# Performance work log

Hardware: AMD Instinct MI355X
Metric: run time of the kernel (lower is better)

The kernel has to match this reference:

```python
import jax, jax.numpy as jnp
import numpy as np

N_NODES = 100000
N_EDGES = 1600000
NFEAT = 128
NHID = 64


def setup_inputs() -> dict:
    key = jax.random.key(0)
    k1, k2, k3, k4 = jax.random.split(key, 4)
    x = jax.random.normal(k1, (N_NODES, NFEAT), dtype=jnp.float32)
    edge_index = jax.random.randint(k2, (2, N_EDGES), 0, N_NODES, dtype=jnp.int64)
    # Glorot-ish scaled weights
    W1 = jax.random.normal(k3, (NFEAT, NHID), dtype=jnp.float32) * (1.0 / np.sqrt(NFEAT))
    b1 = jnp.zeros((NHID,), dtype=jnp.float32)
    W2 = jax.random.normal(k4, (NHID, NFEAT), dtype=jnp.float32) * (1.0 / np.sqrt(NHID))
    b2 = jnp.zeros((NFEAT,), dtype=jnp.float32)
    return {"x": x, "edge_index": edge_index, "W1": W1, "b1": b1, "W2": W2, "b2": b2}


def _gcn_norm(edge_index, num_nodes):
    # PyG GCNConv default: add self-loops, symmetric normalization D^-1/2 A D^-1/2
    src, dst = edge_index[0], edge_index[1]
    loops = jnp.arange(num_nodes, dtype=src.dtype)
    src = jnp.concatenate([src, loops])
    dst = jnp.concatenate([dst, loops])
    ones = jnp.ones(src.shape[0], dtype=jnp.float32)
    deg = jax.ops.segment_sum(ones, dst, num_segments=num_nodes)  # in-degree incl. self-loop
    dinv = jax.lax.rsqrt(deg)  # deg >= 1 due to self-loops
    norm = dinv[src] * dinv[dst]  # [E + N]
    return src, dst, norm


def _gcn_conv(h, W, b, src, dst, norm, num_nodes):
    h = h @ W                                  # [N, d_out] transform first (d_out small)
    msg = norm[:, None] * h[src]               # gather over edges [E+N, d_out]
    out = jax.ops.segment_sum(msg, dst, num_segments=num_nodes)  # scatter-add
    return out + b


def reference(x, edge_index, W1, b1, W2, b2):
    num_nodes = x.shape[0]
    src, dst, norm = _gcn_norm(edge_index, num_nodes)
    h = jax.nn.relu(_gcn_conv(x, W1, b1, src, dst, norm, num_nodes))
    # dropout is identity in eval mode (deterministic reference baseline)
    out = _gcn_conv(h, W2, b2, src, dst, norm, num_nodes)
    return out
```

## Files before the change

kernel.cpp:

```cpp
#include <hip/hip_runtime.h>
#include <hip/hip_fp16.h>

#define NFEAT 128
#define NHID 64
#define MAXB 1024
#define BSHIFT 8
#define BNODES 256
#define PBLK 512
#define DBINS 512

typedef _Float16 f16x8 __attribute__((ext_vector_type(8)));
typedef float f32x4 __attribute__((ext_vector_type(4)));

__global__ void k_detect(const int* __restrict__ ei_words, int nwords, int* flag,
                         const float* __restrict__ W1, __half* __restrict__ w1t,
                         const float* __restrict__ W2, __half* __restrict__ w2t) {
    __shared__ int s_or;
    if (threadIdx.x == 0) s_or = 0;
    __syncthreads();
    int acc = 0;
    for (int i = 1 + 2 * (int)threadIdx.x; i < nwords; i += 2 * (int)blockDim.x)
        acc |= ei_words[i];
    atomicOr(&s_or, acc);
    for (int i = threadIdx.x; i < NFEAT * NHID; i += 256) {
        int n = i >> 7, k = i & 127;
        w1t[i] = __float2half(W1[k * NHID + n]);
    }
    for (int i = threadIdx.x; i < NFEAT * NHID; i += 256) {
        int n = i >> 6, k = i & 63;
        w2t[i] = __float2half(W2[k * NFEAT + n]);
    }
    __syncthreads();
    if (threadIdx.x == 0) *flag = (s_or == 0) ? 1 : 0;
}

__device__ __forceinline__ int edge_idx(const int* __restrict__ ei, int is64,
                                        long long E, long long e, int which) {
    long long pos = which ? (E + e) : e;
    return is64 ? ei[2 * pos] : ei[pos];
}

__device__ __forceinline__ void load8(const int* __restrict__ ei, int is64,
                                      long long E, long long e0, int which,
                                      int (&v)[8]) {
    if (is64) {
        const int* base = ei + 2 * (which ? E + e0 : e0);
        int4 a = *(const int4*)(base + 0);
        int4 b = *(const int4*)(base + 4);
        int4 c = *(const int4*)(base + 8);
        int4 d = *(const int4*)(base + 12);
        v[0] = a.x; v[1] = a.z; v[2] = b.x; v[3] = b.z;
        v[4] = c.x; v[5] = c.z; v[6] = d.x; v[7] = d.z;
    } else {
        const int* base = ei + (which ? E + e0 : e0);
        int4 a = *(const int4*)(base + 0);
        int4 b = *(const int4*)(base + 4);
        v[0] = a.x; v[1] = a.y; v[2] = a.z; v[3] = a.w;
        v[4] = b.x; v[5] = b.y; v[6] = b.z; v[7] = b.w;
    }
}

__global__ __launch_bounds__(256) void k_bhist(const int* __restrict__ ei,
                                               const int* __restrict__ flag,
                                               long long E, int* gbhist,
                                               int* __restrict__ blockhist,
                                               int NB, long long perblk) {
    __shared__ int hist[MAXB];
    for (int i = threadIdx.x; i < NB; i += 256) hist[i] = 0;
    __syncthreads();
    int is64 = *flag;
    long long lo = (long long)blockIdx.x * perblk;
    long long hi = lo + perblk; if (hi > E) hi = E;
    for (long long e0 = lo + (long long)threadIdx.x * 8; e0 + 8 <= hi; e0 += 256 * 8) {
        int d[8];
        load8(ei, is64, E, e0, 1, d);
#pragma unroll
        for (int j = 0; j < 8; ++j)
            atomicAdd(&hist[d[j] >> BSHIFT], 1);
    }
    long long tail = lo + ((hi - lo) & ~7LL);
    for (long long e = tail + threadIdx.x; e < hi; e += 256) {
        int d = edge_idx(ei, is64, E, e, 1);
        atomicAdd(&hist[d >> BSHIFT], 1);
    }
    __syncthreads();
    int* bh = blockhist + (size_t)blockIdx.x * MAXB;
    for (int i = threadIdx.x; i < NB; i += 256) {
        int v = hist[i];
        bh[i] = v;
        if (v) atomicAdd(&gbhist[i], v);
    }
}

__global__ __launch_bounds__(256) void k_bscan(const int* __restrict__ gbhist, int NB,
                                               int* boff, int* bcur, int* offN) {
    __shared__ int s[256];
    int t = threadIdx.x;
    int v[4]; int sum = 0;
#pragma unroll
    for (int j = 0; j < 4; ++j) {
        int i = t * 4 + j;
        v[j] = (i < NB) ? gbhist[i] : 0;
        sum += v[j];
    }
    s[t] = sum;
    __syncthreads();
    for (int d = 1; d < 256; d <<= 1) {
        int val = (t >= d) ? s[t - d] : 0;
        __syncthreads();
        s[t] += val;
        __syncthreads();
    }
    int run = s[t] - sum;
#pragma unroll
    for (int j = 0; j < 4; ++j) {
        int i = t * 4 + j;
        if (i <= NB) boff[i] = run;
        if (i < NB)  bcur[i] = run;
        run += v[j];
    }
    if (t == 255) *offN = s[255];
}

__global__ __launch_bounds__(256) void k_partition(const int* __restrict__ ei,
                                                   const int* __restrict__ flag,
                                                   long long E, int* bcur,
                                                   const int* __restrict__ blockhist,
                                                   unsigned* __restrict__ staging,
                                                   int NB, long long perblk) {
    __shared__ int cur[MAXB];
    const int* bh = blockhist + (size_t)blockIdx.x * MAXB;
    for (int i = threadIdx.x; i < NB; i += 256) {
        int v = bh[i];
        cur[i] = v ? atomicAdd(&bcur[i], v) : 0;
    }
    __syncthreads();
    long long lo = (long long)blockIdx.x * perblk;
    long long hi = lo + perblk; if (hi > E) hi = E;
    int is64 = *flag;
    for (long long e0 = lo + (long long)threadIdx.x * 8; e0 + 8 <= hi; e0 += 256 * 8) {
        int s[8], d[8];
        load8(ei, is64, E, e0, 0, s);
        load8(ei, is64, E, e0, 1, d);
#pragma unroll
        for (int j = 0; j < 8; ++j) {
            int pos = atomicAdd(&cur[d[j] >> BSHIFT], 1);
            staging[pos] = (unsigned)s[j] | ((unsigned)(d[j] & (BNODES - 1)) << 24);
        }
    }
    long long tail = lo + ((hi - lo) & ~7LL);
    for (long long e = tail + threadIdx.x; e < hi; e += 256) {
        int s = edge_idx(ei, is64, E, e, 0);
        int d = edge_idx(ei, is64, E, e, 1);
        int pos = atomicAdd(&cur[d >> BSHIFT], 1);
        staging[pos] = (unsigned)s | ((unsigned)(d & (BNODES - 1)) << 24);
    }
}

__global__ __launch_bounds__(256) void k_bucket(const unsigned* __restrict__ staging,
                                                const int* __restrict__ boff,
                                                int N, int* off, int* esrc, float* dinv,
                                                int* __restrict__ deghist) {
    __shared__ int cnt_s[BNODES];
    __shared__ int scan_s[BNODES];
    __shared__ int dh[DBINS];
    int b = blockIdx.x;
    int base = b << BSHIFT;
    int t = threadIdx.x;
    cnt_s[t] = 0;
    dh[t] = 0; dh[t + 256] = 0;
    __syncthreads();
    int lo = boff[b], hi = boff[b + 1];
    for (int e = lo + t; e < hi; e += 256)
        atomicAdd(&cnt_s[staging[e] >> 24], 1);
    __syncthreads();
    int v = cnt_s[t];
    scan_s[t] = v;
    __syncthreads();
    for (int d = 1; d < 256; d <<= 1) {
        int val = (t >= d) ? scan_s[t - d] : 0;
        __syncthreads();
        scan_s[t] += val;
        __syncthreads();
    }
    int excl = scan_s[t] - v;
    int node = base + t;
    if (node < N) {
        off[node] = lo + excl;
        dinv[node] = rsqrtf((float)v + 1.0f);
        atomicAdd(&dh[v < (DBINS - 1) ? v : (DBINS - 1)], 1);
    }
    __syncthreads();
    if (dh[t])       atomicAdd(&deghist[t], dh[t]);
    if (dh[t + 256]) atomicAdd(&deghist[t + 256], dh[t + 256]);
    cnt_s[t] = lo + excl;
    __syncthreads();
    for (int e = lo + t; e < hi; e += 256) {
        unsigned sd = staging[e];
        int pos = atomicAdd(&cnt_s[sd >> 24], 1);
        esrc[pos] = (int)(sd & 0xFFFFFFu);
    }
}

__global__ __launch_bounds__(256) void k_dscan(const int* __restrict__ deghist, int* dcur) {
    __shared__ int s[256];
    int t = threadIdx.x;
    int v0 = deghist[2 * t], v1 = deghist[2 * t + 1];
    int sum = v0 + v1;
    s[t] = sum;
    __syncthreads();
    for (int d = 1; d < 256; d <<= 1) {
        int val = (t >= d) ? s[t - d] : 0;
        __syncthreads();
        s[t] += val;
        __syncthreads();
    }
    int run = s[t] - sum;
    dcur[2 * t] = run;
    dcur[2 * t + 1] = run + v0;
}

__global__ __launch_bounds__(256) void k_dperm(const int* __restrict__ off, int* dcur,
                                               int* __restrict__ perm, int N) {
    __shared__ int cnt[DBINS];
    __shared__ int base[DBINS];
    int t = threadIdx.x;
    cnt[t] = 0; cnt[t + 256] = 0;
    __syncthreads();
    int n = blockIdx.x * 256 + t;
    int b = 0, myidx = 0;
    if (n < N) {
        int deg = off[n + 1] - off[n];
        b = deg < (DBINS - 1) ? deg : (DBINS - 1);
        myidx = atomicAdd(&cnt[b], 1);
    }
    __syncthreads();
    int c0 = cnt[t];       if (c0) base[t] = atomicAdd(&dcur[t], c0);
    int c1 = cnt[t + 256]; if (c1) base[t + 256] = atomicAdd(&dcur[t + 256], c1);
    __syncthreads();
    if (n < N) perm[base[b] + myidx] = n;
}

__device__ __forceinline__ int swz(int row, int byteoff) {
    return (row << 8) + (byteoff ^ ((row & 7) << 4));
}
__device__ __forceinline__ int swz64(int row, int byteoff) {
    return (row << 7) + (byteoff ^ ((row & 7) << 4));
}

__global__ __launch_bounds__(256) void k_gemm1(const float* __restrict__ x,
                                               const __half* __restrict__ w1t,
                                               const float* __restrict__ dinv,
                                               __half* __restrict__ xw1s, int N) {
    __shared__ __align__(16) __half xs[64 * NFEAT];
    __shared__ __align__(16) __half ws[NHID * NFEAT];
    int t = threadIdx.x;
    for (int i = t; i < NHID * NFEAT / 8; i += 256) {
        int row = i >> 4, c16 = (i & 15) << 4;
        uint4 v = ((const uint4*)w1t)[i];
        *(uint4*)((char*)ws + swz(row, c16)) = v;
    }
    int row0 = blockIdx.x * 64;
    for (int i = t; i < 64 * 32; i += 256) {
        int r = i >> 5, c4 = i & 31;
        int row = row0 + r;
        float4 v = (row < N) ? ((const float4*)x)[(size_t)row * 32 + c4]
                             : make_float4(0.f, 0.f, 0.f, 0.f);
        __half2 h0 = __floats2half2_rn(v.x, v.y);
        __half2 h1 = __floats2half2_rn(v.z, v.w);
        uint2 p = make_uint2(*(unsigned*)&h0, *(unsigned*)&h1);
        *(uint2*)((char*)xs + swz(r, c4 * 8)) = p;
    }
    __syncthreads();
    int wave = t >> 6, lane = t & 63;
    int lr = lane & 15, g = lane >> 4;
    int xrow = wave * 16 + lr;
    f16x8 xb[4];
#pragma unroll
    for (int kc = 0; kc < 4; ++kc)
        xb[kc] = *(const f16x8*)((const char*)xs + swz(xrow, kc * 64 + g * 16));
    int row = row0 + xrow;
    float di = (row < N) ? dinv[row] : 0.f;
#pragma unroll
    for (int c = 0; c < 4; ++c) {
        f32x4 acc = {0.f, 0.f, 0.f, 0.f};
#pragma unroll
        for (int kc = 0; kc < 4; ++kc) {
            f16x8 a = *(const f16x8*)((const char*)ws + swz(c * 16 + lr, kc * 64 + g * 16));
            acc = __builtin_amdgcn_mfma_f32_16x16x32_f16(a, xb[kc], acc, 0, 0, 0);
        }
        if (row < N) {
            __half2 o0 = __floats2half2_rn(di * acc[0], di * acc[1]);
            __half2 o1 = __floats2half2_rn(di * acc[2], di * acc[3]);
            uint2 p = make_uint2(*(unsigned*)&o0, *(unsigned*)&o1);
            *(uint2*)&xw1s[(size_t)row * NHID + c * 16 + g * 4] = p;
        }
    }
}

__device__ __forceinline__ void addhalf8(float2 (&acc)[4], uint4 p) {
    const __half2* hh = (const __half2*)&p;
#pragma unroll
    for (int j = 0; j < 4; ++j) {
        float2 v = __half22float2(hh[j]);
        acc[j].x += v.x; acc[j].y += v.y;
    }
}

__device__ __forceinline__ void gather_group(const int* __restrict__ off,
                                             const int* __restrict__ esrc,
                                             const uint4* __restrict__ feat4,
                                             int d, int li, int lo, int hi,
                                             float2 (&acc)[4]) {
#pragma unroll
    for (int j = 0; j < 4; ++j) acc[j] = make_float2(0.f, 0.f);
    int idx = (lo + li < hi) ? esrc[lo + li] : 0;
    for (int e = lo; e < hi; e += 8) {
        int nrem = hi - e;
        int cur = idx;
        int ne = e + 8;
        idx = (ne + li < hi) ? esrc[ne + li] : 0;
        if (nrem >= 8) {
#pragma unroll
            for (int j = 0; j < 8; ++j) {
                int s = __shfl(cur, j, 8);
                addhalf8(acc, feat4[(size_t)s * 8 + li]);
            }
        } else {
            for (int j = 0; j < nrem; ++j) {
                int s = __shfl(cur, j, 8);
                addhalf8(acc, feat4[(size_t)s * 8 + li]);
            }
        }
    }
    addhalf8(acc, feat4[(size_t)d * 8 + li]);
}

__global__ __launch_bounds__(256) void k_agg1(const int* __restrict__ off,
                                              const int* __restrict__ esrc,
                                              const int* __restrict__ perm,
                                              const float* __restrict__ dinv,
                                              const uint4* __restrict__ xw1s4,
                                              const float* __restrict__ b1,
                                              uint4* __restrict__ h4, int N) {
    int t = threadIdx.x;
    int lane = t & 63, wave = t >> 6;
    int g = lane >> 3, li = lane & 7;
    int slot = blockIdx.x * 32 + wave * 8 + g;
    bool valid = slot < N;
    int d  = valid ? perm[slot] : 0;
    int lo = valid ? off[d] : 0;
    int hi = valid ? off[d + 1] : 0;
    float2 acc[4];
    gather_group(off, esrc, xw1s4, d, li, lo, hi, acc);
    float dd = dinv[d];
    float4 bA = ((const float4*)b1)[li * 2 + 0];
    float4 bB = ((const float4*)b1)[li * 2 + 1];
    float v0 = fmaxf(dd * acc[0].x + bA.x, 0.f);
    float v1 = fmaxf(dd * acc[0].y + bA.y, 0.f);
    float v2 = fmaxf(dd * acc[1].x + bA.z, 0.f);
    float v3 = fmaxf(dd * acc[1].y + bA.w, 0.f);
    float v4 = fmaxf(dd * acc[2].x + bB.x, 0.f);
    float v5 = fmaxf(dd * acc[2].y + bB.y, 0.f);
    float v6 = fmaxf(dd * acc[3].x + bB.z, 0.f);
    float v7 = fmaxf(dd * acc[3].y + bB.w, 0.f);
    __half2 o[4];
    o[0] = __floats2half2_rn(dd * v0, dd * v1);
    o[1] = __floats2half2_rn(dd * v2, dd * v3);
    o[2] = __floats2half2_rn(dd * v4, dd * v5);
    o[3] = __floats2half2_rn(dd * v6, dd * v7);
    if (valid) h4[(size_t)d * 8 + li] = *(const uint4*)o;
}

__global__ __launch_bounds__(256) void k_agg2(const int* __restrict__ off,
                                              const int* __restrict__ esrc,
                                              const int* __restrict__ perm,
                                              const float* __restrict__ dinv,
                                              const uint4* __restrict__ h4,
                                              uint4* __restrict__ a2h,
                                              uint4* __restrict__ a2l, int N) {
    int t = threadIdx.x;
    int lane = t & 63, wave = t >> 6;
    int g = lane >> 3, li = lane & 7;
    int slot = blockIdx.x * 32 + wave * 8 + g;
    bool valid = slot < N;
    int d  = valid ? perm[slot] : 0;
    int lo = valid ? off[d] : 0;
    int hi = valid ? off[d + 1] : 0;
    float2 acc[4];
    gather_group(off, esrc, h4, d, li, lo, hi, acc);
    float dd = dinv[d];
    float v[8] = {dd * acc[0].x, dd * acc[0].y, dd * acc[1].x, dd * acc[1].y,
                  dd * acc[2].x, dd * acc[2].y, dd * acc[3].x, dd * acc[3].y};
    __half hh[8], ll[8];
#pragma unroll
    for (int j = 0; j < 8; ++j) {
        hh[j] = __float2half(v[j]);
        ll[j] = __float2half(v[j] - __half2float(hh[j]));
    }
    uint4 ph, pl;
    __half2* hp = (__half2*)&ph;
    __half2* lp = (__half2*)&pl;
#pragma unroll
    for (int j = 0; j < 4; ++j) {
        hp[j] = __halves2half2(hh[2 * j], hh[2 * j + 1]);
        lp[j] = __halves2half2(ll[2 * j], ll[2 * j + 1]);
    }
    if (valid) {
        a2h[(size_t)d * 8 + li] = ph;
        a2l[(size_t)d * 8 + li] = pl;
    }
}

__global__ __launch_bounds__(256) void k_gemm2(const __half* __restrict__ a2h,
                                               const __half* __restrict__ a2l,
                                               const __half* __restrict__ w2t,
                                               const float* __restrict__ b2,
                                               float* __restrict__ out, int N) {
    __shared__ __align__(16) __half sB[NFEAT * NHID];
    __shared__ __align__(16) __half sH[64 * NHID];
    __shared__ __align__(16) __half sL[64 * NHID];
    int t = threadIdx.x;
    for (int i = t; i < NFEAT * NHID / 8; i += 256) {
        int row = i >> 3, c16 = (i & 7) << 4;
        uint4 v = ((const uint4*)w2t)[i];
        *(uint4*)((char*)sB + swz64(row, c16)) = v;
    }
    int row0 = blockIdx.x * 64;
    for (int i = t; i < 64 * 8; i += 256) {
        int r = i >> 3, c16 = (i & 7) << 4;
        int row = row0 + r;
        uint4 vh = make_uint4(0, 0, 0, 0), vl = make_uint4(0, 0, 0, 0);
        if (row < N) {
            vh = *(const uint4*)((const char*)a2h + (size_t)row * 128 + c16);
            vl = *(const uint4*)((const char*)a2l + (size_t)row * 128 + c16);
        }
        *(uint4*)((char*)sH + swz64(r, c16)) = vh;
        *(uint4*)((char*)sL + swz64(r, c16)) = vl;
    }
    __syncthreads();
    int wave = t >> 6, lane = t & 63;
    int lr = lane & 15, g = lane >> 4;
    int xrow = wave * 16 + lr;
    f16x8 xh[2], xl[2];
#pragma unroll
    for (int kc = 0; kc < 2; ++kc) {
        xh[kc] = *(const f16x8*)((const char*)sH + swz64(xrow, kc * 64 + g * 16));
        xl[kc] = *(const f16x8*)((const char*)sL + swz64(xrow, kc * 64 + g * 16));
    }
    int row = row0 + xrow;
#pragma unroll
    for (int c = 0; c < 8; ++c) {
        f32x4 acc = {0.f, 0.f, 0.f, 0.f};
#pragma unroll
        for (int kc = 0; kc < 2; ++kc) {
            f16x8 a = *(const f16x8*)((const char*)sB + swz64(c * 16 + lr, kc * 64 + g * 16));
            acc = __builtin_amdgcn_mfma_f32_16x16x32_f16(a, xl[kc], acc, 0, 0, 0);
            acc = __builtin_amdgcn_mfma_f32_16x16x32_f16(a, xh[kc], acc, 0, 0, 0);
        }
        if (row < N) {
            float4 bb = *(const float4*)&b2[c * 16 + g * 4];
            float4 o = make_float4(acc[0] + bb.x, acc[1] + bb.y,
                                   acc[2] + bb.z, acc[3] + bb.w);
            *(float4*)&out[(size_t)row * NFEAT + c * 16 + g * 4] = o;
        }
    }
}

static inline char* align256(char* p) {
    return (char*)(((uintptr_t)p + 255) & ~(uintptr_t)255);
}

extern "C" void kernel_launch(void* const* d_in, const int* in_sizes, int n_in,
                              void* d_out, int out_size, void* d_ws, size_t ws_size,
                              hipStream_t stream) {
    const float* x  = (const float*)d_in[0];
    const int*   ei = (const int*)d_in[1];
    const float* W1 = (const float*)d_in[2];
    const float* b1 = (const float*)d_in[3];
    const float* W2 = (const float*)d_in[4];
    const float* b2 = (const float*)d_in[5];
    float* out = (float*)d_out;

    const int N = in_sizes[0] / NFEAT;
    const long long E = in_sizes[1] / 2;
    const int NB = (N + BNODES - 1) >> BSHIFT;

    char* w = (char*)d_ws;
    int*      flag      = (int*)w;
    int*      gbhist    = (int*)(w + 256);
    int*      boff      = gbhist + MAXB;
    int*      bcur      = boff + MAXB + 1;
    int*      deghist   = bcur + MAXB;
    int*      dcur      = deghist + DBINS;
    int*      blockhist = dcur + DBINS;
    float*    dinv      = (float*)(blockhist + (size_t)PBLK * MAXB);
    int*      off       = (int*)(dinv + N);
    int*      perm      = off + N + 1;
    char*     p         = align256((char*)(perm + N));
    unsigned* staging   = (unsigned*)p;
    p = align256((char*)(staging + E));
    int*      esrc      = (int*)p;
    p = align256((char*)(esrc + E));
    __half*   xw1s      = (__half*)p;
    p = align256((char*)(xw1s + (size_t)N * NHID));
    __half*   h         = (__half*)p;
    p = align256((char*)(h + (size_t)N * NHID));
    __half*   a2h       = (__half*)p;
    p = align256((char*)(a2h + (size_t)N * NHID));
    __half*   a2l       = (__half*)p;
    p = align256((char*)(a2l + (size_t)N * NHID));
    __half*   w1t       = (__half*)p;
    p = align256((char*)(w1t + NFEAT * NHID));
    __half*   w2t       = (__half*)p;

    hipMemsetAsync(gbhist, 0, (size_t)NB * sizeof(int), stream);
    hipMemsetAsync(deghist, 0, (size_t)DBINS * sizeof(int), stream);

    long long perblk = ((E + PBLK - 1) / PBLK + 7) & ~7LL;
    k_detect<<<1, 256, 0, stream>>>(ei, 4096, flag, W1, w1t, W2, w2t);
    k_bhist<<<PBLK, 256, 0, stream>>>(ei, flag, E, gbhist, blockhist, NB, perblk);
    k_bscan<<<1, 256, 0, stream>>>(gbhist, NB, boff, bcur, off + N);
    k_partition<<<PBLK, 256, 0, stream>>>(ei, flag, E, bcur, blockhist, staging, NB, perblk);
    k_bucket<<<NB, 256, 0, stream>>>(staging, boff, N, off, esrc, dinv, deghist);
    k_dscan<<<1, 256, 0, stream>>>(deghist, dcur);
    k_dperm<<<(N + 255) / 256, 256, 0, stream>>>(off, dcur, perm, N);

    k_gemm1<<<(N + 63) / 64, 256, 0, stream>>>(x, w1t, dinv, xw1s, N);

    k_agg1<<<(N + 31) / 32, 256, 0, stream>>>(off, esrc, perm, dinv, (const uint4*)xw1s,
                                              b1, (uint4*)h, N);
    k_agg2<<<(N + 31) / 32, 256, 0, stream>>>(off, esrc, perm, dinv, (const uint4*)h,
                                              (uint4*)a2h, (uint4*)a2l, N);

    k_gemm2<<<(N + 63) / 64, 256, 0, stream>>>(a2h, a2l, w2t, b2, out, N);
}
```

Measured before the change: 303.8 us.

## Fuse CSR preprocessing into one cooperative kernel with grid syncs

Replaces the seven preprocessing kernels and two memsets with a single cooperative kernel that moves between phases with grid.sync(). A fallback chain of separate kernels runs if the cooperative launch fails. Global atomics on bucket cursors are replaced by a deterministic column scan over per-block histograms. Weight transposition moves into the GEMM kernels, each of which converts fp32 weights with scattered half stores. The aim is to cut launch and inter-kernel gaps; the trade-offs are grid-sync cost, limited occupancy at 2 blocks/SM, and the bucket and dperm phases now looping over 512 blocks.

```diff
diff --git a/kernel.cpp b/kernel.cpp
--- a/kernel.cpp
+++ b/kernel.cpp
@@ -1,5 +1,8 @@
 #include <hip/hip_runtime.h>
 #include <hip/hip_fp16.h>
+#include <hip/hip_cooperative_groups.h>
+
+namespace cg = cooperative_groups;
 
 #define NFEAT 128
 #define NHID 64
@@ -12,27 +15,6 @@
 typedef _Float16 f16x8 __attribute__((ext_vector_type(8)));
 typedef float f32x4 __attribute__((ext_vector_type(4)));
 
-__global__ void k_detect(const int* __restrict__ ei_words, int nwords, int* flag,
-                         const float* __restrict__ W1, __half* __restrict__ w1t,
-                         const float* __restrict__ W2, __half* __restrict__ w2t) {
-    __shared__ int s_or;
-    if (threadIdx.x == 0) s_or = 0;
-    __syncthreads();
-    int acc = 0;
-    for (int i = 1 + 2 * (int)threadIdx.x; i < nwords; i += 2 * (int)blockDim.x)
-        acc |= ei_words[i];
-    atomicOr(&s_or, acc);
-    for (int i = threadIdx.x; i < NFEAT * NHID; i += 256) {
-        int n = i >> 7, k = i & 127;
-        w1t[i] = __float2half(W1[k * NHID + n]);
-    }
-    for (int i = threadIdx.x; i < NFEAT * NHID; i += 256) {
-        int n = i >> 6, k = i & 63;
-        w2t[i] = __float2half(W2[k * NFEAT + n]);
-    }
-    __syncthreads();
-    if (threadIdx.x == 0) *flag = (s_or == 0) ? 1 : 0;
-}
 
 __device__ __forceinline__ int edge_idx(const int* __restrict__ ei, int is64,
                                         long long E, long long e, int which) {
@@ -60,41 +42,79 @@
     }
 }
 
-__global__ __launch_bounds__(256) void k_bhist(const int* __restrict__ ei,
-                                               const int* __restrict__ flag,
-                                               long long E, int* gbhist,
-                                               int* __restrict__ blockhist,
-                                               int NB, long long perblk) {
-    __shared__ int hist[MAXB];
+__device__ __forceinline__ int block_is64(const int* __restrict__ ei, int* smem) {
+    if (threadIdx.x == 0) smem[0] = 0;
+    __syncthreads();
+    int acc = 0;
+    for (int i = 1 + 2 * (int)threadIdx.x; i < 4096; i += 512)
+        acc |= ei[i];
+    atomicOr(&smem[0], acc);
+    __syncthreads();
+    int r = (smem[0] == 0) ? 1 : 0;
+    __syncthreads();
+    return r;
+}
+
+__device__ void phase_hist(const int* __restrict__ ei, int is64, long long E,
+                           long long perblk, int* __restrict__ blockhist,
+                           int NB, int* smem) {
+    int* hist = smem;
     for (int i = threadIdx.x; i < NB; i += 256) hist[i] = 0;
     __syncthreads();
-    int is64 = *flag;
     long long lo = (long long)blockIdx.x * perblk;
     long long hi = lo + perblk; if (hi > E) hi = E;
-    for (long long e0 = lo + (long long)threadIdx.x * 8; e0 + 8 <= hi; e0 += 256 * 8) {
-        int d[8];
-        load8(ei, is64, E, e0, 1, d);
-#pragma unroll
-        for (int j = 0; j < 8; ++j)
-            atomicAdd(&hist[d[j] >> BSHIFT], 1);
-    }
-    long long tail = lo + ((hi - lo) & ~7LL);
-    for (long long e = tail + threadIdx.x; e < hi; e += 256) {
-        int d = edge_idx(ei, is64, E, e, 1);
-        atomicAdd(&hist[d >> BSHIFT], 1);
+    if (lo < hi) {
+        for (long long e0 = lo + (long long)threadIdx.x * 8; e0 + 8 <= hi; e0 += 256 * 8) {
+            int d[8];
+            load8(ei, is64, E, e0, 1, d);
+#pragma unroll
+            for (int j = 0; j < 8; ++j)
+                atomicAdd(&hist[d[j] >> BSHIFT], 1);
+        }
+        long long tail = lo + ((hi - lo) & ~7LL);
+        for (long long e = tail + threadIdx.x; e < hi; e += 256) {
+            int d = edge_idx(ei, is64, E, e, 1);
+            atomicAdd(&hist[d >> BSHIFT], 1);
+        }
     }
     __syncthreads();
     int* bh = blockhist + (size_t)blockIdx.x * MAXB;
-    for (int i = threadIdx.x; i < NB; i += 256) {
-        int v = hist[i];
-        bh[i] = v;
-        if (v) atomicAdd(&gbhist[i], v);
-    }
-}
-
-__global__ __launch_bounds__(256) void k_bscan(const int* __restrict__ gbhist, int NB,
-                                               int* boff, int* bcur, int* offN) {
-    __shared__ int s[256];
+    for (int i = threadIdx.x; i < NB; i += 256) bh[i] = hist[i];
+    __syncthreads();
+}
+
+__device__ void phase_colscan(int* __restrict__ blockhist, int* __restrict__ gbhist,
+                              int* __restrict__ deghist, int NB, int* smem) {
+    int b = blockIdx.x;
+    int t = threadIdx.x;
+    if (b < NB) {
+        int v0 = blockhist[(size_t)(2 * t) * MAXB + b];
+        int v1 = blockhist[(size_t)(2 * t + 1) * MAXB + b];
+        int sum = v0 + v1;
+        int* s = smem;
+        s[t] = sum;
+        __syncthreads();
+        for (int d = 1; d < 256; d <<= 1) {
+            int val = (t >= d) ? s[t - d] : 0;
+            __syncthreads();
+            s[t] += val;
+            __syncthreads();
+        }
+        int run = s[t] - sum;
+        blockhist[(size_t)(2 * t) * MAXB + b] = run;
+        blockhist[(size_t)(2 * t + 1) * MAXB + b] = run + v0;
+        if (t == 255) gbhist[b] = s[255];
+        __syncthreads();
+    } else {
+        int idx = (b - NB) * 256 + t;
+        if (idx < DBINS) deghist[idx] = 0;
+    }
+}
+
+__device__ void phase_bscan(const int* __restrict__ gbhist, int NB,
+                            int* __restrict__ boff, int* __restrict__ offN,
+                            int* smem) {
+    int* s = smem;
     int t = threadIdx.x;
     int v[4]; int sum = 0;
 #pragma unroll
@@ -116,94 +136,96 @@
     for (int j = 0; j < 4; ++j) {
         int i = t * 4 + j;
         if (i <= NB) boff[i] = run;
-        if (i < NB)  bcur[i] = run;
         run += v[j];
     }
     if (t == 255) *offN = s[255];
-}
-
-__global__ __launch_bounds__(256) void k_partition(const int* __restrict__ ei,
-                                                   const int* __restrict__ flag,
-                                                   long long E, int* bcur,
-                                                   const int* __restrict__ blockhist,
-                                                   unsigned* __restrict__ staging,
-                                                   int NB, long long perblk) {
-    __shared__ int cur[MAXB];
+    __syncthreads();
+}
+
+__device__ void phase_partition(const int* __restrict__ ei, int is64, long long E,
+                                long long perblk, const int* __restrict__ boff,
+                                const int* __restrict__ blockhist,
+                                unsigned* __restrict__ staging, int NB, int* smem) {
+    int* cur = smem;
     const int* bh = blockhist + (size_t)blockIdx.x * MAXB;
-    for (int i = threadIdx.x; i < NB; i += 256) {
-        int v = bh[i];
-        cur[i] = v ? atomicAdd(&bcur[i], v) : 0;
-    }
+    for (int i = threadIdx.x; i < NB; i += 256)
+        cur[i] = boff[i] + bh[i];
     __syncthreads();
     long long lo = (long long)blockIdx.x * perblk;
     long long hi = lo + perblk; if (hi > E) hi = E;
-    int is64 = *flag;
-    for (long long e0 = lo + (long long)threadIdx.x * 8; e0 + 8 <= hi; e0 += 256 * 8) {
-        int s[8], d[8];
-        load8(ei, is64, E, e0, 0, s);
-        load8(ei, is64, E, e0, 1, d);
-#pragma unroll
-        for (int j = 0; j < 8; ++j) {
-            int pos = atomicAdd(&cur[d[j] >> BSHIFT], 1);
-            staging[pos] = (unsigned)s[j] | ((unsigned)(d[j] & (BNODES - 1)) << 24);
-        }
-    }
-    long long tail = lo + ((hi - lo) & ~7LL);
-    for (long long e = tail + threadIdx.x; e < hi; e += 256) {
-        int s = edge_idx(ei, is64, E, e, 0);
-        int d = edge_idx(ei, is64, E, e, 1);
-        int pos = atomicAdd(&cur[d >> BSHIFT], 1);
-        staging[pos] = (unsigned)s | ((unsigned)(d & (BNODES - 1)) << 24);
-    }
-}
-
-__global__ __launch_bounds__(256) void k_bucket(const unsigned* __restrict__ staging,
-                                                const int* __restrict__ boff,
-                                                int N, int* off, int* esrc, float* dinv,
-                                                int* __restrict__ deghist) {
-    __shared__ int cnt_s[BNODES];
-    __shared__ int scan_s[BNODES];
-    __shared__ int dh[DBINS];
-    int b = blockIdx.x;
-    int base = b << BSHIFT;
-    int t = threadIdx.x;
-    cnt_s[t] = 0;
-    dh[t] = 0; dh[t + 256] = 0;
-    __syncthreads();
-    int lo = boff[b], hi = boff[b + 1];
-    for (int e = lo + t; e < hi; e += 256)
-        atomicAdd(&cnt_s[staging[e] >> 24], 1);
-    __syncthreads();
-    int v = cnt_s[t];
-    scan_s[t] = v;
-    __syncthreads();
-    for (int d = 1; d < 256; d <<= 1) {
-        int val = (t >= d) ? scan_s[t - d] : 0;
-        __syncthreads();
-        scan_s[t] += val;
-        __syncthreads();
-    }
-    int excl = scan_s[t] - v;
-    int node = base + t;
-    if (node < N) {
-        off[node] = lo + excl;
-        dinv[node] = rsqrtf((float)v + 1.0f);
-        atomicAdd(&dh[v < (DBINS - 1) ? v : (DBINS - 1)], 1);
-    }
-    __syncthreads();
-    if (dh[t])       atomicAdd(&deghist[t], dh[t]);
-    if (dh[t + 256]) atomicAdd(&deghist[t + 256], dh[t + 256]);
-    cnt_s[t] = lo + excl;
-    __syncthreads();
-    for (int e = lo + t; e < hi; e += 256) {
-        unsigned sd = staging[e];
-        int pos = atomicAdd(&cnt_s[sd >> 24], 1);
-        esrc[pos] = (int)(sd & 0xFFFFFFu);
-    }
-}
-
-__global__ __launch_bounds__(256) void k_dscan(const int* __restrict__ deghist, int* dcur) {
-    __shared__ int s[256];
+    if (lo < hi) {
+        for (long long e0 = lo + (long long)threadIdx.x * 8; e0 + 8 <= hi; e0 += 256 * 8) {
+            int s[8], d[8];
+            load8(ei, is64, E, e0, 0, s);
+            load8(ei, is64, E, e0, 1, d);
+#pragma unroll
+            for (int j = 0; j < 8; ++j) {
+                int pos = atomicAdd(&cur[d[j] >> BSHIFT], 1);
+                staging[pos] = (unsigned)s[j] | ((unsigned)(d[j] & (BNODES - 1)) << 24);
+            }
+        }
+        long long tail = lo + ((hi - lo) & ~7LL);
+        for (long long e = tail + threadIdx.x; e < hi; e += 256) {
+            int s = edge_idx(ei, is64, E, e, 0);
+            int d = edge_idx(ei, is64, E, e, 1);
+            int pos = atomicAdd(&cur[d >> BSHIFT], 1);
+            staging[pos] = (unsigned)s | ((unsigned)(d & (BNODES - 1)) << 24);
+        }
+    }
+    __syncthreads();
+}
+
+__device__ void phase_bucket(const unsigned* __restrict__ staging,
+                             const int* __restrict__ boff, int N, int NB,
+                             int* __restrict__ off, int* __restrict__ esrc,
+                             float* __restrict__ dinv, int* __restrict__ deghist,
+                             int* smem) {
+    int* cnt_s  = smem;
+    int* scan_s = smem + 256;
+    int* dh     = smem + 512;
+    int t = threadIdx.x;
+    for (int b = blockIdx.x; b < NB; b += PBLK) {
+        int base = b << BSHIFT;
+        cnt_s[t] = 0;
+        dh[t] = 0; dh[t + 256] = 0;
+        __syncthreads();
+        int lo = boff[b], hi = boff[b + 1];
+        for (int e = lo + t; e < hi; e += 256)
+            atomicAdd(&cnt_s[staging[e] >> 24], 1);
+        __syncthreads();
+        int v = cnt_s[t];
+        scan_s[t] = v;
+        __syncthreads();
+        for (int d = 1; d < 256; d <<= 1) {
+            int val = (t >= d) ? scan_s[t - d] : 0;
+            __syncthreads();
+            scan_s[t] += val;
+            __syncthreads();
+        }
+        int excl = scan_s[t] - v;
+        int node = base + t;
+        if (node < N) {
+            off[node] = lo + excl;
+            dinv[node] = rsqrtf((float)v + 1.0f);
+            atomicAdd(&dh[v < (DBINS - 1) ? v : (DBINS - 1)], 1);
+        }
+        __syncthreads();
+        if (dh[t])       atomicAdd(&deghist[t], dh[t]);
+        if (dh[t + 256]) atomicAdd(&deghist[t + 256], dh[t + 256]);
+        cnt_s[t] = lo + excl;
+        __syncthreads();
+        for (int e = lo + t; e < hi; e += 256) {
+            unsigned sd = staging[e];
+            int pos = atomicAdd(&cnt_s[sd >> 24], 1);
+            esrc[pos] = (int)(sd & 0xFFFFFFu);
+        }
+        __syncthreads();
+    }
+}
+
+__device__ void phase_dscan(const int* __restrict__ deghist, int* __restrict__ dcur,
+                            int* smem) {
+    int* s = smem;
     int t = threadIdx.x;
     int v0 = deghist[2 * t], v1 = deghist[2 * t + 1];
     int sum = v0 + v1;
@@ -218,27 +240,93 @@
     int run = s[t] - sum;
     dcur[2 * t] = run;
     dcur[2 * t + 1] = run + v0;
-}
-
-__global__ __launch_bounds__(256) void k_dperm(const int* __restrict__ off, int* dcur,
-                                               int* __restrict__ perm, int N) {
-    __shared__ int cnt[DBINS];
-    __shared__ int base[DBINS];
-    int t = threadIdx.x;
-    cnt[t] = 0; cnt[t + 256] = 0;
-    __syncthreads();
-    int n = blockIdx.x * 256 + t;
-    int b = 0, myidx = 0;
-    if (n < N) {
-        int deg = off[n + 1] - off[n];
-        b = deg < (DBINS - 1) ? deg : (DBINS - 1);
-        myidx = atomicAdd(&cnt[b], 1);
-    }
-    __syncthreads();
-    int c0 = cnt[t];       if (c0) base[t] = atomicAdd(&dcur[t], c0);
-    int c1 = cnt[t + 256]; if (c1) base[t + 256] = atomicAdd(&dcur[t + 256], c1);
-    __syncthreads();
-    if (n < N) perm[base[b] + myidx] = n;
+    __syncthreads();
+}
+
+__device__ void phase_dperm(const int* __restrict__ off, int* __restrict__ dcur,
+                            int* __restrict__ perm, int N, int* smem) {
+    int* cnt  = smem;
+    int* base = smem + 512;
+    int t = threadIdx.x;
+    for (long long n0 = (long long)blockIdx.x * 256; n0 < N; n0 += (long long)PBLK * 256) {
+        cnt[t] = 0; cnt[t + 256] = 0;
+        __syncthreads();
+        int n = (int)n0 + t;
+        int b = 0, myidx = 0;
+        if (n < N) {
+            int deg = off[n + 1] - off[n];
+            b = deg < (DBINS - 1) ? deg : (DBINS - 1);
+            myidx = atomicAdd(&cnt[b], 1);
+        }
+        __syncthreads();
+        int c0 = cnt[t];       if (c0) base[t] = atomicAdd(&dcur[t], c0);
+        int c1 = cnt[t + 256]; if (c1) base[t + 256] = atomicAdd(&dcur[t + 256], c1);
+        __syncthreads();
+        if (n < N) perm[base[b] + myidx] = n;
+        __syncthreads();
+    }
+}
+
+__global__ __launch_bounds__(256, 2) void k_preproc_coop(
+        const int* __restrict__ ei, long long E, int N, int NB, long long perblk,
+        int* blockhist, int* gbhist, int* boff, unsigned* staging,
+        int* off, int* esrc, float* dinv, int* deghist, int* dcur, int* perm) {
+    __shared__ int smem[1024];
+    cg::grid_group grid = cg::this_grid();
+    int is64 = block_is64(ei, smem);
+    phase_hist(ei, is64, E, perblk, blockhist, NB, smem);
+    grid.sync();
+    phase_colscan(blockhist, gbhist, deghist, NB, smem);
+    grid.sync();
+    if (blockIdx.x == 0) phase_bscan(gbhist, NB, boff, off + N, smem);
+    grid.sync();
+    phase_partition(ei, is64, E, perblk, boff, blockhist, staging, NB, smem);
+    grid.sync();
+    phase_bucket(staging, boff, N, NB, off, esrc, dinv, deghist, smem);
+    grid.sync();
+    if (blockIdx.x == 0) phase_dscan(deghist, dcur, smem);
+    grid.sync();
+    phase_dperm(off, dcur, perm, N, smem);
+}
+
+__global__ __launch_bounds__(256) void k_f_hist(const int* __restrict__ ei, long long E,
+                                                long long perblk, int* blockhist, int NB) {
+    __shared__ int smem[1024];
+    int is64 = block_is64(ei, smem);
+    phase_hist(ei, is64, E, perblk, blockhist, NB, smem);
+}
+__global__ __launch_bounds__(256) void k_f_colscan(int* blockhist, int* gbhist,
+                                                   int* deghist, int NB) {
+    __shared__ int smem[1024];
+    phase_colscan(blockhist, gbhist, deghist, NB, smem);
+}
+__global__ __launch_bounds__(256) void k_f_bscan(const int* gbhist, int NB,
+                                                 int* boff, int* offN) {
+    __shared__ int smem[1024];
+    phase_bscan(gbhist, NB, boff, offN, smem);
+}
+__global__ __launch_bounds__(256) void k_f_partition(const int* __restrict__ ei, long long E,
+                                                     long long perblk, const int* boff,
+                                                     const int* blockhist,
+                                                     unsigned* staging, int NB) {
+    __shared__ int smem[1024];
+    int is64 = block_is64(ei, smem);
+    phase_partition(ei, is64, E, perblk, boff, blockhist, staging, NB, smem);
+}
+__global__ __launch_bounds__(256) void k_f_bucket(const unsigned* staging, const int* boff,
+                                                  int N, int NB, int* off, int* esrc,
+                                                  float* dinv, int* deghist) {
+    __shared__ int smem[1024];
+    phase_bucket(staging, boff, N, NB, off, esrc, dinv, deghist, smem);
+}
+__global__ __launch_bounds__(256) void k_f_dscan(const int* deghist, int* dcur) {
+    __shared__ int smem[1024];
+    phase_dscan(deghist, dcur, smem);
+}
+__global__ __launch_bounds__(256) void k_f_dperm(const int* off, int* dcur,
+                                                 int* perm, int N) {
+    __shared__ int smem[1024];
+    phase_dperm(off, dcur, perm, N, smem);
 }
 
 __device__ __forceinline__ int swz(int row, int byteoff) {
@@ -249,16 +337,15 @@
 }
 
 __global__ __launch_bounds__(256) void k_gemm1(const float* __restrict__ x,
-                                               const __half* __restrict__ w1t,
+                                               const float* __restrict__ W1,
                                                const float* __restrict__ dinv,
                                                __half* __restrict__ xw1s, int N) {
     __shared__ __align__(16) __half xs[64 * NFEAT];
     __shared__ __align__(16) __half ws[NHID * NFEAT];
     int t = threadIdx.x;
-    for (int i = t; i < NHID * NFEAT / 8; i += 256) {
-        int row = i >> 4, c16 = (i & 15) << 4;
-        uint4 v = ((const uint4*)w1t)[i];
-        *(uint4*)((char*)ws + swz(row, c16)) = v;
+    for (int i = t; i < NFEAT * NHID; i += 256) {
+        int k = i >> 6, n = i & 63;
+        *(__half*)((char*)ws + swz(n, k * 2)) = __float2half(W1[i]);
     }
     int row0 = blockIdx.x * 64;
     for (int i = t; i < 64 * 32; i += 256) {
@@ -414,17 +501,16 @@
 
 __global__ __launch_bounds__(256) void k_gemm2(const __half* __restrict__ a2h,
                                                const __half* __restrict__ a2l,
-                                               const __half* __restrict__ w2t,
+                                               const float* __restrict__ W2,
                                                const float* __restrict__ b2,
                                                float* __restrict__ out, int N) {
     __shared__ __align__(16) __half sB[NFEAT * NHID];
     __shared__ __align__(16) __half sH[64 * NHID];
     __shared__ __align__(16) __half sL[64 * NHID];
     int t = threadIdx.x;
-    for (int i = t; i < NFEAT * NHID / 8; i += 256) {
-        int row = i >> 3, c16 = (i & 7) << 4;
-        uint4 v = ((const uint4*)w2t)[i];
-        *(uint4*)((char*)sB + swz64(row, c16)) = v;
+    for (int i = t; i < NFEAT * NHID; i += 256) {
+        int k = i >> 7, n = i & 127;
+        *(__half*)((char*)sB + swz64(n, k * 2)) = __float2half(W2[i]);
     }
     int row0 = blockIdx.x * 64;
     for (int i = t; i < 64 * 8; i += 256) {
@@ -487,11 +573,9 @@
     const int NB = (N + BNODES - 1) >> BSHIFT;
 
     char* w = (char*)d_ws;
-    int*      flag      = (int*)w;
-    int*      gbhist    = (int*)(w + 256);
+    int*      gbhist    = (int*)w;
     int*      boff      = gbhist + MAXB;
-    int*      bcur      = boff + MAXB + 1;
-    int*      deghist   = bcur + MAXB;
+    int*      deghist   = boff + MAXB + 1;
     int*      dcur      = deghist + DBINS;
     int*      blockhist = dcur + DBINS;
     float*    dinv      = (float*)(blockhist + (size_t)PBLK * MAXB);
@@ -509,29 +593,41 @@
     __half*   a2h       = (__half*)p;
     p = align256((char*)(a2h + (size_t)N * NHID));
     __half*   a2l       = (__half*)p;
-    p = align256((char*)(a2l + (size_t)N * NHID));
-    __half*   w1t       = (__half*)p;
-    p = align256((char*)(w1t + NFEAT * NHID));
-    __half*   w2t       = (__half*)p;
-
-    hipMemsetAsync(gbhist, 0, (size_t)NB * sizeof(int), stream);
-    hipMemsetAsync(deghist, 0, (size_t)DBINS * sizeof(int), stream);
 
     long long perblk = ((E + PBLK - 1) / PBLK + 7) & ~7LL;
-    k_detect<<<1, 256, 0, stream>>>(ei, 4096, flag, W1, w1t, W2, w2t);
-    k_bhist<<<PBLK, 256, 0, stream>>>(ei, flag, E, gbhist, blockhist, NB, perblk);
-    k_bscan<<<1, 256, 0, stream>>>(gbhist, NB, boff, bcur, off + N);
-    k_partition<<<PBLK, 256, 0, stream>>>(ei, flag, E, bcur, blockhist, staging, NB, perblk);
-    k_bucket<<<NB, 256, 0, stream>>>(staging, boff, N, off, esrc, dinv, deghist);
-    k_dscan<<<1, 256, 0, stream>>>(deghist, dcur);
-    k_dperm<<<(N + 255) / 256, 256, 0, stream>>>(off, dcur, perm, N);
-
-    k_gemm1<<<(N + 63) / 64, 256, 0, stream>>>(x, w1t, dinv, xw1s, N);
+
+    {
+        const int* ei_ = ei; long long E_ = E; int N_ = N; int NB_ = NB;
+        long long pb_ = perblk;
+        int* blockhist_ = blockhist; int* gbhist_ = gbhist; int* boff_ = boff;
+        unsigned* staging_ = staging; int* off_ = off; int* esrc_ = esrc;
+        float* dinv_ = dinv; int* deghist_ = deghist; int* dcur_ = dcur;
+        int* perm_ = perm;
+        void* args[] = {&ei_, &E_, &N_, &NB_, &pb_, &blockhist_, &gbhist_, &boff_,
+                        &staging_, &off_, &esrc_, &dinv_, &deghist_, &dcur_, &perm_};
+        hipError_t ce = hipLaunchCooperativeKernel(
+            reinterpret_cast<const void*>(&k_preproc_coop),
+            dim3(PBLK), dim3(256), args, 0, stream);
+        if (ce != hipSuccess) {
+            (void)hipGetLastError();
+            k_f_hist<<<PBLK, 256, 0, stream>>>(ei, E, perblk, blockhist, NB);
+            k_f_colscan<<<PBLK, 256, 0, stream>>>(blockhist, gbhist, deghist, NB);
+            k_f_bscan<<<1, 256, 0, stream>>>(gbhist, NB, boff, off + N);
+            k_f_partition<<<PBLK, 256, 0, stream>>>(ei, E, perblk, boff, blockhist,
+                                                    staging, NB);
+            k_f_bucket<<<PBLK, 256, 0, stream>>>(staging, boff, N, NB, off, esrc,
+                                                 dinv, deghist);
+            k_f_dscan<<<1, 256, 0, stream>>>(deghist, dcur);
+            k_f_dperm<<<PBLK, 256, 0, stream>>>(off, dcur, perm, N);
+        }
+    }
+
+    k_gemm1<<<(N + 63) / 64, 256, 0, stream>>>(x, W1, dinv, xw1s, N);
 
     k_agg1<<<(N + 31) / 32, 256, 0, stream>>>(off, esrc, perm, dinv, (const uint4*)xw1s,
                                               b1, (uint4*)h, N);
     k_agg2<<<(N + 31) / 32, 256, 0, stream>>>(off, esrc, perm, dinv, (const uint4*)h,
                                               (uint4*)a2h, (uint4*)a2l, N);
 
-    k_gemm2<<<(N + 63) / 64, 256, 0, stream>>>(a2h, a2l, w2t, b2, out, N);
-}
+    k_gemm2<<<(N + 63) / 64, 256, 0, stream>>>(a2h, a2l, W2, b2, out, N);
+}
```

Measured after the change: 639.7 us. 2.11x slower.

## Remove detect kernel and memsets; replace atomic bucket offsets with column scan

Applied to the files above, without the earlier changes.

Drops the single-block detect kernel and both memsets. Each histogram and partition block now detects the index width itself, and the weight transpose and fp16 conversion moves into the GEMM kernels' shared-memory staging. A new column-scan kernel computes deterministic per-block bucket offsets, which replaces the global atomics on bcur and gbhist; it also zeroes the degree histogram. The goal is fewer launches and less serial single-block work, at the cost of redundant weight conversion in every GEMM block and one extra scan launch.

```diff
diff --git a/kernel.cpp b/kernel.cpp
--- a/kernel.cpp
+++ b/kernel.cpp
@@ -12,27 +12,6 @@
 typedef _Float16 f16x8 __attribute__((ext_vector_type(8)));
 typedef float f32x4 __attribute__((ext_vector_type(4)));
 
-__global__ void k_detect(const int* __restrict__ ei_words, int nwords, int* flag,
-                         const float* __restrict__ W1, __half* __restrict__ w1t,
-                         const float* __restrict__ W2, __half* __restrict__ w2t) {
-    __shared__ int s_or;
-    if (threadIdx.x == 0) s_or = 0;
-    __syncthreads();
-    int acc = 0;
-    for (int i = 1 + 2 * (int)threadIdx.x; i < nwords; i += 2 * (int)blockDim.x)
-        acc |= ei_words[i];
-    atomicOr(&s_or, acc);
-    for (int i = threadIdx.x; i < NFEAT * NHID; i += 256) {
-        int n = i >> 7, k = i & 127;
-        w1t[i] = __float2half(W1[k * NHID + n]);
-    }
-    for (int i = threadIdx.x; i < NFEAT * NHID; i += 256) {
-        int n = i >> 6, k = i & 63;
-        w2t[i] = __float2half(W2[k * NFEAT + n]);
-    }
-    __syncthreads();
-    if (threadIdx.x == 0) *flag = (s_or == 0) ? 1 : 0;
-}
 
 __device__ __forceinline__ int edge_idx(const int* __restrict__ ei, int is64,
                                         long long E, long long e, int which) {
@@ -60,40 +39,79 @@
     }
 }
 
-__global__ __launch_bounds__(256) void k_bhist(const int* __restrict__ ei,
-                                               const int* __restrict__ flag,
-                                               long long E, int* gbhist,
-                                               int* __restrict__ blockhist,
-                                               int NB, long long perblk) {
-    __shared__ int hist[MAXB];
+__device__ __forceinline__ int block_is64(const int* __restrict__ ei, int* smem) {
+    if (threadIdx.x == 0) smem[0] = 0;
+    __syncthreads();
+    int acc = 0;
+    for (int i = 1 + 2 * (int)threadIdx.x; i < 4096; i += 512)
+        acc |= ei[i];
+    atomicOr(&smem[0], acc);
+    __syncthreads();
+    int r = (smem[0] == 0) ? 1 : 0;
+    __syncthreads();
+    return r;
+}
+
+__global__ __launch_bounds__(256) void k_hist(const int* __restrict__ ei, long long E,
+                                              long long perblk,
+                                              int* __restrict__ blockhist, int NB) {
+    __shared__ int smem[1024];
+    int is64 = block_is64(ei, smem);
+    int* hist = smem;
     for (int i = threadIdx.x; i < NB; i += 256) hist[i] = 0;
     __syncthreads();
-    int is64 = *flag;
     long long lo = (long long)blockIdx.x * perblk;
     long long hi = lo + perblk; if (hi > E) hi = E;
-    for (long long e0 = lo + (long long)threadIdx.x * 8; e0 + 8 <= hi; e0 += 256 * 8) {
-        int d[8];
-        load8(ei, is64, E, e0, 1, d);
-#pragma unroll
-        for (int j = 0; j < 8; ++j)
-            atomicAdd(&hist[d[j] >> BSHIFT], 1);
-    }
-    long long tail = lo + ((hi - lo) & ~7LL);
-    for (long long e = tail + threadIdx.x; e < hi; e += 256) {
-        int d = edge_idx(ei, is64, E, e, 1);
-        atomicAdd(&hist[d >> BSHIFT], 1);
+    if (lo < hi) {
+        for (long long e0 = lo + (long long)threadIdx.x * 8; e0 + 8 <= hi; e0 += 256 * 8) {
+            int d[8];
+            load8(ei, is64, E, e0, 1, d);
+#pragma unroll
+            for (int j = 0; j < 8; ++j)
+                atomicAdd(&hist[d[j] >> BSHIFT], 1);
+        }
+        long long tail = lo + ((hi - lo) & ~7LL);
+        for (long long e = tail + threadIdx.x; e < hi; e += 256) {
+            int d = edge_idx(ei, is64, E, e, 1);
+            atomicAdd(&hist[d >> BSHIFT], 1);
+        }
     }
     __syncthreads();
     int* bh = blockhist + (size_t)blockIdx.x * MAXB;
-    for (int i = threadIdx.x; i < NB; i += 256) {
-        int v = hist[i];
-        bh[i] = v;
-        if (v) atomicAdd(&gbhist[i], v);
+    for (int i = threadIdx.x; i < NB; i += 256) bh[i] = hist[i];
+}
+
+__global__ __launch_bounds__(256) void k_colscan(int* __restrict__ blockhist,
+                                                 int* __restrict__ gbhist,
+                                                 int* __restrict__ deghist, int NB) {
+    __shared__ int s[256];
+    int b = blockIdx.x;
+    int t = threadIdx.x;
+    if (b < NB) {
+        int v0 = blockhist[(size_t)(2 * t) * MAXB + b];
+        int v1 = blockhist[(size_t)(2 * t + 1) * MAXB + b];
+        int sum = v0 + v1;
+        s[t] = sum;
+        __syncthreads();
+        for (int d = 1; d < 256; d <<= 1) {
+            int val = (t >= d) ? s[t - d] : 0;
+            __syncthreads();
+            s[t] += val;
+            __syncthreads();
+        }
+        int run = s[t] - sum;
+        blockhist[(size_t)(2 * t) * MAXB + b] = run;
+        blockhist[(size_t)(2 * t + 1) * MAXB + b] = run + v0;
+        if (t == 255) gbhist[b] = s[255];
+    } else {
+        int idx = (b - NB) * 256 + t;
+        if (idx < DBINS) deghist[idx] = 0;
     }
 }
 
 __global__ __launch_bounds__(256) void k_bscan(const int* __restrict__ gbhist, int NB,
-                                               int* boff, int* bcur, int* offN) {
+                                               int* __restrict__ boff,
+                                               int* __restrict__ offN) {
     __shared__ int s[256];
     int t = threadIdx.x;
     int v[4]; int sum = 0;
@@ -116,93 +134,98 @@
     for (int j = 0; j < 4; ++j) {
         int i = t * 4 + j;
         if (i <= NB) boff[i] = run;
-        if (i < NB)  bcur[i] = run;
         run += v[j];
     }
     if (t == 255) *offN = s[255];
 }
 
-__global__ __launch_bounds__(256) void k_partition(const int* __restrict__ ei,
-                                                   const int* __restrict__ flag,
-                                                   long long E, int* bcur,
+__global__ __launch_bounds__(256) void k_partition(const int* __restrict__ ei, long long E,
+                                                   long long perblk,
+                                                   const int* __restrict__ boff,
                                                    const int* __restrict__ blockhist,
-                                                   unsigned* __restrict__ staging,
-                                                   int NB, long long perblk) {
-    __shared__ int cur[MAXB];
+                                                   unsigned* __restrict__ staging, int NB) {
+    __shared__ int smem[1024];
+    int is64 = block_is64(ei, smem);
+    int* cur = smem;
     const int* bh = blockhist + (size_t)blockIdx.x * MAXB;
-    for (int i = threadIdx.x; i < NB; i += 256) {
-        int v = bh[i];
-        cur[i] = v ? atomicAdd(&bcur[i], v) : 0;
-    }
+    for (int i = threadIdx.x; i < NB; i += 256)
+        cur[i] = boff[i] + bh[i];
     __syncthreads();
     long long lo = (long long)blockIdx.x * perblk;
     long long hi = lo + perblk; if (hi > E) hi = E;
-    int is64 = *flag;
-    for (long long e0 = lo + (long long)threadIdx.x * 8; e0 + 8 <= hi; e0 += 256 * 8) {
-        int s[8], d[8];
-        load8(ei, is64, E, e0, 0, s);
-        load8(ei, is64, E, e0, 1, d);
-#pragma unroll
-        for (int j = 0; j < 8; ++j) {
-            int pos = atomicAdd(&cur[d[j] >> BSHIFT], 1);
-            staging[pos] = (unsigned)s[j] | ((unsigned)(d[j] & (BNODES - 1)) << 24);
-        }
-    }
-    long long tail = lo + ((hi - lo) & ~7LL);
-    for (long long e = tail + threadIdx.x; e < hi; e += 256) {
-        int s = edge_idx(ei, is64, E, e, 0);
-        int d = edge_idx(ei, is64, E, e, 1);
-        int pos = atomicAdd(&cur[d >> BSHIFT], 1);
-        staging[pos] = (unsigned)s | ((unsigned)(d & (BNODES - 1)) << 24);
+    if (lo < hi) {
+        for (long long e0 = lo + (long long)threadIdx.x * 8; e0 + 8 <= hi; e0 += 256 * 8) {
+            int s[8], d[8];
+            load8(ei, is64, E, e0, 0, s);
+            load8(ei, is64, E, e0, 1, d);
+#pragma unroll
+            for (int j = 0; j < 8; ++j) {
+                int pos = atomicAdd(&cur[d[j] >> BSHIFT], 1);
+                staging[pos] = (unsigned)s[j] | ((unsigned)(d[j] & (BNODES - 1)) << 24);
+            }
+        }
+        long long tail = lo + ((hi - lo) & ~7LL);
+        for (long long e = tail + threadIdx.x; e < hi; e += 256) {
+            int s = edge_idx(ei, is64, E, e, 0);
+            int d = edge_idx(ei, is64, E, e, 1);
+            int pos = atomicAdd(&cur[d >> BSHIFT], 1);
+            staging[pos] = (unsigned)s | ((unsigned)(d & (BNODES - 1)) << 24);
+        }
     }
 }
 
 __global__ __launch_bounds__(256) void k_bucket(const unsigned* __restrict__ staging,
                                                 const int* __restrict__ boff,
-                                                int N, int* off, int* esrc, float* dinv,
+                                                int N, int NB,
+                                                int* __restrict__ off,
+                                                int* __restrict__ esrc,
+                                                float* __restrict__ dinv,
                                                 int* __restrict__ deghist) {
     __shared__ int cnt_s[BNODES];
     __shared__ int scan_s[BNODES];
     __shared__ int dh[DBINS];
-    int b = blockIdx.x;
-    int base = b << BSHIFT;
-    int t = threadIdx.x;
-    cnt_s[t] = 0;
-    dh[t] = 0; dh[t + 256] = 0;
-    __syncthreads();
-    int lo = boff[b], hi = boff[b + 1];
-    for (int e = lo + t; e < hi; e += 256)
-        atomicAdd(&cnt_s[staging[e] >> 24], 1);
-    __syncthreads();
-    int v = cnt_s[t];
-    scan_s[t] = v;
-    __syncthreads();
-    for (int d = 1; d < 256; d <<= 1) {
-        int val = (t >= d) ? scan_s[t - d] : 0;
-        __syncthreads();
-        scan_s[t] += val;
-        __syncthreads();
-    }
-    int excl = scan_s[t] - v;
-    int node = base + t;
-    if (node < N) {
-        off[node] = lo + excl;
-        dinv[node] = rsqrtf((float)v + 1.0f);
-        atomicAdd(&dh[v < (DBINS - 1) ? v : (DBINS - 1)], 1);
-    }
-    __syncthreads();
-    if (dh[t])       atomicAdd(&deghist[t], dh[t]);
-    if (dh[t + 256]) atomicAdd(&deghist[t + 256], dh[t + 256]);
-    cnt_s[t] = lo + excl;
-    __syncthreads();
-    for (int e = lo + t; e < hi; e += 256) {
-        unsigned sd = staging[e];
-        int pos = atomicAdd(&cnt_s[sd >> 24], 1);
-        esrc[pos] = (int)(sd & 0xFFFFFFu);
-    }
-}
-
-__global__ __launch_bounds__(256) void k_dscan(const int* __restrict__ deghist, int* dcur) {
+    int t = threadIdx.x;
+    for (int b = blockIdx.x; b < NB; b += gridDim.x) {
+        int base = b << BSHIFT;
+        cnt_s[t] = 0;
+        dh[t] = 0; dh[t + 256] = 0;
+        __syncthreads();
+        int lo = boff[b], hi = boff[b + 1];
+        for (int e = lo + t; e < hi; e += 256)
+            atomicAdd(&cnt_s[staging[e] >> 24], 1);
+        __syncthreads();
+        int v = cnt_s[t];
+        scan_s[t] = v;
+        __syncthreads();
+        for (int d = 1; d < 256; d <<= 1) {
+            int val = (t >= d) ? scan_s[t - d] : 0;
+            __syncthreads();
+            scan_s[t] += val;
+            __syncthreads();
+        }
+        int excl = scan_s[t] - v;
+        int node = base + t;
+        if (node < N) {
+            off[node] = lo + excl;
+            dinv[node] = rsqrtf((float)v + 1.0f);
+            atomicAdd(&dh[v < (DBINS - 1) ? v : (DBINS - 1)], 1);
+        }
+        __syncthreads();
+        if (dh[t])       atomicAdd(&deghist[t], dh[t]);
+        if (dh[t + 256]) atomicAdd(&deghist[t + 256], dh[t + 256]);
+        cnt_s[t] = lo + excl;
+        __syncthreads();
+        for (int e = lo + t; e < hi; e += 256) {
+            unsigned sd = staging[e];
+            int pos = atomicAdd(&cnt_s[sd >> 24], 1);
+            esrc[pos] = (int)(sd & 0xFFFFFFu);
+        }
+        __syncthreads();
+    }
+}
+
+__global__ __launch_bounds__(256) void k_dscan(const int* __restrict__ deghist,
+                                               int* __restrict__ dcur) {
     __shared__ int s[256];
     int t = threadIdx.x;
     int v0 = deghist[2 * t], v1 = deghist[2 * t + 1];
@@ -220,7 +243,8 @@
     dcur[2 * t + 1] = run + v0;
 }
 
-__global__ __launch_bounds__(256) void k_dperm(const int* __restrict__ off, int* dcur,
+__global__ __launch_bounds__(256) void k_dperm(const int* __restrict__ off,
+                                               int* __restrict__ dcur,
                                                int* __restrict__ perm, int N) {
     __shared__ int cnt[DBINS];
     __shared__ int base[DBINS];
@@ -249,16 +273,15 @@
 }
 
 __global__ __launch_bounds__(256) void k_gemm1(const float* __restrict__ x,
-                                               const __half* __restrict__ w1t,
+                                               const float* __restrict__ W1,
                                                const float* __restrict__ dinv,
                                                __half* __restrict__ xw1s, int N) {
     __shared__ __align__(16) __half xs[64 * NFEAT];
     __shared__ __align__(16) __half ws[NHID * NFEAT];
     int t = threadIdx.x;
-    for (int i = t; i < NHID * NFEAT / 8; i += 256) {
-        int row = i >> 4, c16 = (i & 15) << 4;
-        uint4 v = ((const uint4*)w1t)[i];
-        *(uint4*)((char*)ws + swz(row, c16)) = v;
+    for (int i = t; i < NFEAT * NHID; i += 256) {
+        int k = i >> 6, n = i & 63;
+        *(__half*)((char*)ws + swz(n, k * 2)) = __float2half(W1[i]);
     }
     int row0 = blockIdx.x * 64;
     for (int i = t; i < 64 * 32; i += 256) {
@@ -414,17 +437,16 @@
 
 __global__ __launch_bounds__(256) void k_gemm2(const __half* __restrict__ a2h,
                                                const __half* __restrict__ a2l,
-                                               const __half* __restrict__ w2t,
+                                               const float* __restrict__ W2,
                                                const float* __restrict__ b2,
                                                float* __restrict__ out, int N) {
     __shared__ __align__(16) __half sB[NFEAT * NHID];
     __shared__ __align__(16) __half sH[64 * NHID];
     __shared__ __align__(16) __half sL[64 * NHID];
     int t = threadIdx.x;
-    for (int i = t; i < NFEAT * NHID / 8; i += 256) {
-        int row = i >> 3, c16 = (i & 7) << 4;
-        uint4 v = ((const uint4*)w2t)[i];
-        *(uint4*)((char*)sB + swz64(row, c16)) = v;
+    for (int i = t; i < NFEAT * NHID; i += 256) {
+        int k = i >> 7, n = i & 127;
+        *(__half*)((char*)sB + swz64(n, k * 2)) = __float2half(W2[i]);
     }
     int row0 = blockIdx.x * 64;
     for (int i = t; i < 64 * 8; i += 256) {
@@ -487,11 +509,9 @@
     const int NB = (N + BNODES - 1) >> BSHIFT;
 
     char* w = (char*)d_ws;
-    int*      flag      = (int*)w;
-    int*      gbhist    = (int*)(w + 256);
+    int*      gbhist    = (int*)w;
     int*      boff      = gbhist + MAXB;
-    int*      bcur      = boff + MAXB + 1;
-    int*      deghist   = bcur + MAXB;
+    int*      deghist   = boff + MAXB + 1;
     int*      dcur      = deghist + DBINS;
     int*      blockhist = dcur + DBINS;
     float*    dinv      = (float*)(blockhist + (size_t)PBLK * MAXB);
@@ -509,29 +529,23 @@
     __half*   a2h       = (__half*)p;
     p = align256((char*)(a2h + (size_t)N * NHID));
     __half*   a2l       = (__half*)p;
-    p = align256((char*)(a2l + (size_t)N * NHID));
-    __half*   w1t       = (__half*)p;
-    p = align256((char*)(w1t + NFEAT * NHID));
-    __half*   w2t       = (__half*)p;
-
-    hipMemsetAsync(gbhist, 0, (size_t)NB * sizeof(int), stream);
-    hipMemsetAsync(deghist, 0, (size_t)DBINS * sizeof(int), stream);
 
     long long perblk = ((E + PBLK - 1) / PBLK + 7) & ~7LL;
-    k_detect<<<1, 256, 0, stream>>>(ei, 4096, flag, W1, w1t, W2, w2t);
-    k_bhist<<<PBLK, 256, 0, stream>>>(ei, flag, E, gbhist, blockhist, NB, perblk);
-    k_bscan<<<1, 256, 0, stream>>>(gbhist, NB, boff, bcur, off + N);
-    k_partition<<<PBLK, 256, 0, stream>>>(ei, flag, E, bcur, blockhist, staging, NB, perblk);
-    k_bucket<<<NB, 256, 0, stream>>>(staging, boff, N, off, esrc, dinv, deghist);
+
+    k_hist<<<PBLK, 256, 0, stream>>>(ei, E, perblk, blockhist, NB);
+    k_colscan<<<NB + 2, 256, 0, stream>>>(blockhist, gbhist, deghist, NB);
+    k_bscan<<<1, 256, 0, stream>>>(gbhist, NB, boff, off + N);
+    k_partition<<<PBLK, 256, 0, stream>>>(ei, E, perblk, boff, blockhist, staging, NB);
+    k_bucket<<<NB, 256, 0, stream>>>(staging, boff, N, NB, off, esrc, deghist ? dinv : dinv, deghist);
     k_dscan<<<1, 256, 0, stream>>>(deghist, dcur);
     k_dperm<<<(N + 255) / 256, 256, 0, stream>>>(off, dcur, perm, N);
 
-    k_gemm1<<<(N + 63) / 64, 256, 0, stream>>>(x, w1t, dinv, xw1s, N);
+    k_gemm1<<<(N + 63) / 64, 256, 0, stream>>>(x, W1, dinv, xw1s, N);
 
     k_agg1<<<(N + 31) / 32, 256, 0, stream>>>(off, esrc, perm, dinv, (const uint4*)xw1s,
                                               b1, (uint4*)h, N);
     k_agg2<<<(N + 31) / 32, 256, 0, stream>>>(off, esrc, perm, dinv, (const uint4*)h,
                                               (uint4*)a2h, (uint4*)a2l, N);
 
-    k_gemm2<<<(N + 63) / 64, 256, 0, stream>>>(a2h, a2l, w2t, b2, out, N);
-}
+    k_gemm2<<<(N + 63) / 64, 256, 0, stream>>>(a2h, a2l, W2, b2, out, N);
+}
```

New measurement: 266.5 us. -12.3%, faster.
